# Kernel tuning notes

Hardware: AMD Instinct MI355X
Metric: run time of the kernel (lower is better)

Reference implementation:

```python
import jax, jax.numpy as jnp
import numpy as np

N_NODES = 500_000
N_EDGES = 16_000_000


def setup_inputs() -> dict:
    key = jax.random.key(0)
    ks = jax.random.split(key, 8)
    x = jax.random.normal(ks[0], (N_NODES, 10), dtype=jnp.float32)
    edge_index = jax.random.randint(ks[1], (2, N_EDGES), 0, N_NODES, dtype=jnp.int32)
    # PyG-style init scale ~ 1/sqrt(fan_in)
    Wl1 = jax.random.normal(ks[2], (5, 10), dtype=jnp.float32) / np.sqrt(10)
    Wr1 = jax.random.normal(ks[3], (5, 10), dtype=jnp.float32) / np.sqrt(10)
    b1 = jnp.zeros((5,), jnp.float32)
    Wl_mid = jax.random.normal(ks[4], (8, 5, 5), dtype=jnp.float32) / np.sqrt(5)
    Wr_mid = jax.random.normal(ks[5], (8, 5, 5), dtype=jnp.float32) / np.sqrt(5)
    b_mid = jnp.zeros((8, 5), jnp.float32)
    Wl10 = jax.random.normal(ks[6], (1, 5), dtype=jnp.float32) / np.sqrt(5)
    Wr10 = jax.random.normal(ks[7], (1, 5), dtype=jnp.float32) / np.sqrt(5)
    b10 = jnp.zeros((1,), jnp.float32)
    return dict(x=x, edge_index=edge_index, Wl1=Wl1, Wr1=Wr1, b1=b1,
                Wl_mid=Wl_mid, Wr_mid=Wr_mid, b_mid=b_mid,
                Wl10=Wl10, Wr10=Wr10, b10=b10)


def _mean_aggregate(h, src, dst):
    # scatter-mean of source features onto destination nodes
    s = jax.ops.segment_sum(h[src], dst, num_segments=N_NODES)
    cnt = jax.ops.segment_sum(jnp.ones((src.shape[0], 1), h.dtype), dst,
                              num_segments=N_NODES)
    return s / jnp.maximum(cnt, 1.0)


def _sage_conv(h, src, dst, Wl, Wr, b):
    # out = lin_l(mean_neighbors) + lin_r(h); bias belongs to lin_l (PyG default)
    agg = _mean_aggregate(h, src, dst)
    return agg @ Wl.T + h @ Wr.T + b


def reference(x, edge_index, Wl1, Wr1, b1, Wl_mid, Wr_mid, b_mid, Wl10, Wr10, b10):
    src, dst = edge_index[0], edge_index[1]
    h = jax.nn.relu(_sage_conv(x, src, dst, Wl1, Wr1, b1))

    def step(h, layer_params):
        Wl, Wr, b = layer_params
        h = jax.nn.relu(_sage_conv(h, src, dst, Wl, Wr, b))
        return h, None

    h, _ = jax.lax.scan(step, h, (Wl_mid, Wr_mid, b_mid))
    out = _sage_conv(h, src, dst, Wl10, Wr10, b10)  # [N, 1], no relu on last
    return out
```

## Files before the change

kernel.cpp:

```cpp
#include <hip/hip_runtime.h>

constexpr int NN = 500000;
constexpr int NE = 16000000;
constexpr int BN = 512;
constexpr int NBUCK = (NN + BN - 1) / BN;
constexpr int NSLICE = 8;
constexpr int NKEY = NSLICE * BN;
constexpr int CAPA = 17408;
constexpr int PAIR_CAP = 5120;
constexpr int TILE_A = 16384;
constexpr int NTILE_A = (NE + TILE_A - 1) / TILE_A;
constexpr int NB_NODE = (NN + 255) / 256;

typedef int int4v __attribute__((ext_vector_type(4)));

__device__ __forceinline__ unsigned bfr(float x) {
    unsigned u = __float_as_uint(x);
    u += 0x7fffu + ((u >> 16) & 1u);
    return u >> 16;
}
__device__ __forceinline__ float bfl(unsigned u) { return __uint_as_float(u << 16); }
__device__ __forceinline__ float bfh(unsigned u) { return __uint_as_float(u & 0xffff0000u); }

__global__ void __launch_bounds__(1024, 8) passA(const int* __restrict__ src,
                                                 const int* __restrict__ dst,
                                                 int* __restrict__ gcnt,
                                                 int* __restrict__ storeA) {
    __shared__ int hist[1024];
    __shared__ int lbase[1024];
    __shared__ int lcur[1024];
    __shared__ int gbase[1024];
    __shared__ int stage[TILE_A];
    const int tid = threadIdx.x;
    const int base = blockIdx.x * TILE_A;
    const int nt = min(TILE_A, NE - base);
    hist[tid] = 0;
    __syncthreads();
    for (int i = tid; i < nt; i += 1024)
        atomicAdd(&hist[dst[base + i] >> 9], 1);
    __syncthreads();
    const int cnt = hist[tid];
    lbase[tid] = cnt;
    __syncthreads();
    for (int off = 1; off < 1024; off <<= 1) {
        int add = (tid >= off) ? lbase[tid - off] : 0;
        __syncthreads();
        lbase[tid] += add;
        __syncthreads();
    }
    const int lb = lbase[tid] - cnt;
    lcur[tid] = lb;
    if (tid < NBUCK && cnt > 0) {
        int g = atomicAdd(&gcnt[tid], cnt);
        gbase[tid] = tid * CAPA + g;
    }
    __syncthreads();
    lbase[tid] = lb;
    for (int i = tid; i < nt; i += 1024) {
        int d = dst[base + i];
        int s = src[base + i];
        int p = atomicAdd(&lcur[d >> 9], 1);
        stage[p] = (s << 9) | (d & 511);
    }
    __syncthreads();
    const int wid = tid >> 6, lane = tid & 63;
    for (int b = wid; b < NBUCK; b += 16) {
        int c = hist[b];
        if (c == 0) continue;
        int l0 = lbase[b];
        int g0 = gbase[b];
        int wl = min(c, (b + 1) * CAPA - g0);
        for (int j = lane; j < wl; j += 64)
            storeA[g0 + j] = stage[l0 + j];
    }
}

__global__ void __launch_bounds__(512) passB(const int* __restrict__ gcnt,
                                             const int* __restrict__ storeA,
                                             int* __restrict__ sortedB,
                                             float* __restrict__ inv,
                                             int* __restrict__ soff) {
    __shared__ int hist[NKEY];
    __shared__ int sc[512];
    __shared__ int stage[CAPA];
    const int bkt = blockIdx.x;
    const int tid = threadIdx.x;
#pragma unroll
    for (int u = 0; u < NKEY / 512; ++u) hist[tid + u * 512] = 0;
    __syncthreads();
    const int n = min(gcnt[bkt], CAPA);
    const int* bs = storeA + (size_t)bkt * CAPA;
    const int n4 = n & ~3;
    for (int k = tid * 4; k < n4; k += 2048) {
        int4v e4 = *(const int4v*)(bs + k);
#pragma unroll
        for (int u = 0; u < 4; ++u) {
            int e = e4[u];
            int key = ((e >> 26) << 10) | ((e & 511) << 1) | ((e >> 25) & 1);
            atomicAdd(&hist[key], 1);
        }
    }
    for (int k = n4 + tid; k < n; k += 512) {
        int e = bs[k];
        int key = ((e >> 26) << 10) | ((e & 511) << 1) | ((e >> 25) & 1);
        atomicAdd(&hist[key], 1);
    }
    __syncthreads();
    {
        int node = bkt * BN + tid;
        if (node < NN) {
            int c = 0;
#pragma unroll
            for (int p = 0; p < 4; ++p)
#pragma unroll
                for (int q = 0; q < 2; ++q)
                    c += hist[(p << 10) | (tid << 1) | q];
            inv[node] = 1.0f / fmaxf((float)c, 1.0f);
        }
    }
    int v[NKEY / 512];
    int sum = 0;
#pragma unroll
    for (int u = 0; u < NKEY / 512; ++u) {
        v[u] = hist[tid * (NKEY / 512) + u];
        sum += v[u];
    }
    sc[tid] = sum;
    __syncthreads();
    for (int off = 1; off < 512; off <<= 1) {
        int add = (tid >= off) ? sc[tid - off] : 0;
        __syncthreads();
        sc[tid] += add;
        __syncthreads();
    }
    int run = sc[tid] - sum;
    if ((tid & 127) == 0) soff[bkt * 9 + (tid >> 7)] = bkt * CAPA + run;
    if (tid == 511) soff[bkt * 9 + 4] = bkt * CAPA + n;
#pragma unroll
    for (int u = 0; u < NKEY / 512; ++u) {
        hist[tid * (NKEY / 512) + u] = run;
        run += v[u];
    }
    __syncthreads();
    for (int k = tid * 4; k < n4; k += 2048) {
        int4v e4 = *(const int4v*)(bs + k);
#pragma unroll
        for (int u = 0; u < 4; ++u) {
            int e = e4[u];
            int key = ((e >> 26) << 10) | ((e & 511) << 1) | ((e >> 25) & 1);
            int p = atomicAdd(&hist[key], 1);
            stage[p] = e;
        }
    }
    for (int k = n4 + tid; k < n; k += 512) {
        int e = bs[k];
        int key = ((e >> 26) << 10) | ((e & 511) << 1) | ((e >> 25) & 1);
        int p = atomicAdd(&hist[key], 1);
        stage[p] = e;
    }
    __syncthreads();
    int* ob = sortedB + (size_t)bkt * CAPA;
    for (int k = tid * 4; k < n4; k += 2048)
        *(int4v*)(ob + k) = *(const int4v*)(stage + k);
    for (int k = n4 + tid; k < n; k += 512)
        ob[k] = stage[k];
}

__global__ void __launch_bounds__(256) transform0(const float* __restrict__ x,
                                                  const float* __restrict__ Wl1,
                                                  uint4* __restrict__ t16) {
    int i = blockIdx.x * 256 + threadIdx.x;
    if (i >= NN) return;
    float xi[10];
#pragma unroll
    for (int k = 0; k < 10; ++k) xi[k] = x[i * 10 + k];
    float v[5];
#pragma unroll
    for (int j = 0; j < 5; ++j) {
        float a = 0.f;
#pragma unroll
        for (int k = 0; k < 10; ++k) a += xi[k] * Wl1[j * 10 + k];
        v[j] = a;
    }
    uint4 w;
    w.x = bfr(v[0]) | (bfr(v[1]) << 16);
    w.y = bfr(v[2]) | (bfr(v[3]) << 16);
    w.z = bfr(v[4]);
    w.w = 0;
    t16[i] = w;
}

__device__ __forceinline__ void process_range5_lds(const int* eds,
                                                   int k, const int ke,
                                                   const uint4* __restrict__ t16,
                                                   float* __restrict__ acc) {
    int cur = -1;
    float a0 = 0, a1 = 0, a2 = 0, a3 = 0, a4 = 0;
    auto flush = [&]() {
        if (cur >= 0) {
            float* p = &acc[cur * 5];
            atomicAdd(p + 0, a0); atomicAdd(p + 1, a1); atomicAdd(p + 2, a2);
            atomicAdd(p + 3, a3); atomicAdd(p + 4, a4);
        }
    };
    auto edge = [&](int e, uint4 w) {
        int d = e & 511;
        if (d != cur) { flush(); cur = d; a0 = a1 = a2 = a3 = a4 = 0.f; }
        a0 += bfl(w.x); a1 += bfh(w.x); a2 += bfl(w.y); a3 += bfh(w.y); a4 += bfl(w.z);
    };
    while (k < ke && (k & 3)) {
        int e = eds[k];
        edge(e, t16[e >> 9]);
        ++k;
    }
    for (; k + 3 < ke; k += 4) {
        int4v e4 = *(const int4v*)(eds + k);
        uint4 w0 = t16[e4.x >> 9];
        uint4 w1 = t16[e4.y >> 9];
        uint4 w2 = t16[e4.z >> 9];
        uint4 w3 = t16[e4.w >> 9];
        edge(e4.x, w0); edge(e4.y, w1); edge(e4.z, w2); edge(e4.w, w3);
    }
    for (; k < ke; ++k) {
        int e = eds[k];
        edge(e, t16[e >> 9]);
    }
    flush();
}

template <int FIN, int FNEXT>
__global__ void __launch_bounds__(512, 8) layer_fused(const int* __restrict__ soff,
                                                      const int* __restrict__ sorted,
                                                      const uint4* __restrict__ t16,
                                                      const float* __restrict__ hin,
                                                      const float* __restrict__ Wr,
                                                      const float* __restrict__ b,
                                                      const float* __restrict__ Wln,
                                                      const float* __restrict__ inv,
                                                      float* __restrict__ hout,
                                                      uint4* __restrict__ tn16,
                                                      float* __restrict__ tnP) {
    __shared__ float acc[BN * 5];
    __shared__ int eds[PAIR_CAP];
    const int bkt = blockIdx.x;
    const int tid = threadIdx.x;
    for (int k = tid; k < BN * 5; k += 512) acc[k] = 0.f;
#pragma unroll
    for (int p = 0; p < 4; ++p) {
        const int beg = soff[bkt * 9 + p];
        const int n = min(soff[bkt * 9 + p + 1] - beg, PAIR_CAP);
#pragma unroll 4
        for (int k = tid; k < n; k += 512)
            eds[k] = __builtin_nontemporal_load(sorted + beg + k);
        __syncthreads();
        const int c = (n + 511) >> 9;
        const int k = tid * c;
        const int ke = min(k + c, n);
        if (k < ke) process_range5_lds(eds, k, ke, t16, acc);
        __syncthreads();
    }

    int node = bkt * BN + tid;
    if (node >= NN) return;
    float iv = inv[node];
    float vin[FIN];
#pragma unroll
    for (int kk = 0; kk < FIN; ++kk) vin[kk] = hin[(size_t)node * FIN + kk];
    float ho[5];
#pragma unroll
    for (int jo = 0; jo < 5; ++jo) {
        float v = acc[tid * 5 + jo] * iv + b[jo];
#pragma unroll
        for (int kk = 0; kk < FIN; ++kk) v += vin[kk] * Wr[jo * FIN + kk];
        v = fmaxf(v, 0.f);
        hout[(size_t)node * 5 + jo] = v;
        ho[jo] = v;
    }
    if constexpr (FNEXT == 5) {
        float tv[5];
#pragma unroll
        for (int j2 = 0; j2 < 5; ++j2) {
            float v = 0.f;
#pragma unroll
            for (int jo = 0; jo < 5; ++jo) v += ho[jo] * Wln[j2 * 5 + jo];
            tv[j2] = v;
        }
        uint4 w;
        w.x = bfr(tv[0]) | (bfr(tv[1]) << 16);
        w.y = bfr(tv[2]) | (bfr(tv[3]) << 16);
        w.z = bfr(tv[4]);
        w.w = 0;
        tn16[node] = w;
    } else {
        float v = 0.f;
#pragma unroll
        for (int jo = 0; jo < 5; ++jo) v += ho[jo] * Wln[jo];
        tnP[node] = v;
    }
}

__global__ void __launch_bounds__(512, 4) final_layer(const int* __restrict__ soff,
                                                      const int* __restrict__ sorted,
                                                      const float* __restrict__ t,
                                                      const float* __restrict__ hin,
                                                      const float* __restrict__ Wr,
                                                      const float* __restrict__ b,
                                                      const float* __restrict__ inv,
                                                      float* __restrict__ out) {
    __shared__ float acc[BN];
    __shared__ int eds[CAPA];
    const int bkt = blockIdx.x;
    const int tid = threadIdx.x;
    const int base = bkt * CAPA;
    const int n = soff[bkt * 9 + 4] - base;
    if (tid < BN) acc[tid] = 0.f;
    const int sn4 = n & ~3;
    for (int k = tid * 4; k < sn4; k += 2048)
        *(int4v*)(eds + k) = __builtin_nontemporal_load((const int4v*)(sorted + base + k));
    for (int k = sn4 + tid; k < n; k += 512)
        eds[k] = sorted[base + k];
    __syncthreads();
    int c = (n + 511) >> 9;
    int k = tid * c;
    const int ke = min(k + c, n);
    int cur = -1;
    float a0 = 0.f;
    auto flush = [&]() { if (cur >= 0) atomicAdd(&acc[cur], a0); };
    auto edge = [&](int e, float q) {
        int d = e & 511;
        if (d != cur) { flush(); cur = d; a0 = 0.f; }
        a0 += q;
    };
    int kk = k;
    while (kk < ke && (kk & 3)) { int e = eds[kk]; edge(e, t[e >> 9]); ++kk; }
    for (; kk + 3 < ke; kk += 4) {
        int4v e4 = *(const int4v*)(eds + kk);
        float q0 = t[e4.x >> 9], q1 = t[e4.y >> 9], q2 = t[e4.z >> 9], q3 = t[e4.w >> 9];
        edge(e4.x, q0); edge(e4.y, q1); edge(e4.z, q2); edge(e4.w, q3);
    }
    for (; kk < ke; ++kk) { int e = eds[kk]; edge(e, t[e >> 9]); }
    flush();
    __syncthreads();
    int node = bkt * BN + tid;
    if (node >= NN) return;
    float v = acc[tid] * inv[node] + b[0];
#pragma unroll
    for (int kq = 0; kq < 5; ++kq) v += hin[(size_t)node * 5 + kq] * Wr[kq];
    out[node] = v;
}

extern "C" void kernel_launch(void* const* d_in, const int* in_sizes, int n_in,
                              void* d_out, int out_size, void* d_ws, size_t ws_size,
                              hipStream_t stream) {
    (void)in_sizes; (void)n_in; (void)out_size; (void)ws_size;
    const float* x    = (const float*)d_in[0];
    const int*   ei   = (const int*)d_in[1];
    const float* Wl1  = (const float*)d_in[2];
    const float* Wr1  = (const float*)d_in[3];
    const float* b1   = (const float*)d_in[4];
    const float* Wlm  = (const float*)d_in[5];
    const float* Wrm  = (const float*)d_in[6];
    const float* bm   = (const float*)d_in[7];
    const float* Wl10 = (const float*)d_in[8];
    const float* Wr10 = (const float*)d_in[9];
    const float* b10  = (const float*)d_in[10];
    float* out = (float*)d_out;

    const int* src = ei;
    const int* dst = ei + NE;

    int* wsI = (int*)d_ws;
    int*   gcnt    = wsI;
    int*   soff    = wsI + 1024;
    int*   sortedB = wsI + 10240;
    float* inv     = (float*)(wsI + 17017856);
    int*   storeA  = wsI + 20019200;
    uint4* tA = (uint4*)(wsI + 20019200);
    uint4* tB = (uint4*)(wsI + 22019200);
    float* tP = (float*)(wsI + 24019200);
    float* hA = (float*)(wsI + 24519424);
    float* hB = (float*)(wsI + 27020032);

    dim3 gb(NBUCK);
    dim3 tb(512);

    hipMemsetAsync(gcnt, 0, 1024 * sizeof(int), stream);
    passA<<<dim3(NTILE_A), dim3(1024), 0, stream>>>(src, dst, gcnt, storeA);
    passB<<<gb, tb, 0, stream>>>(gcnt, storeA, sortedB, inv, soff);

    transform0<<<dim3(NB_NODE), dim3(256), 0, stream>>>(x, Wl1, tA);
    layer_fused<10, 5><<<gb, tb, 0, stream>>>(soff, sortedB, tA,
                                              x, Wr1, b1, Wlm, inv, hA, tB, nullptr);

    const uint4* tcur = tB; uint4* tnxt = tA;
    const float* hcur = hA; float* hnext = hB;
    for (int mi = 0; mi < 7; ++mi) {
        layer_fused<5, 5><<<gb, tb, 0, stream>>>(soff, sortedB, tcur,
                                                 hcur, Wrm + mi * 25, bm + mi * 5,
                                                 Wlm + (mi + 1) * 25, inv, hnext,
                                                 tnxt, nullptr);
        const uint4* tt = tcur; tcur = tnxt; tnxt = (uint4*)tt;
        const float* th = hcur; hcur = hnext; hnext = (float*)th;
    }
    layer_fused<5, 1><<<gb, tb, 0, stream>>>(soff, sortedB, tcur,
                                             hcur, Wrm + 7 * 25, bm + 7 * 5,
                                             Wl10, inv, hnext, nullptr, tP);
    final_layer<<<gb, tb, 0, stream>>>(soff, sortedB, tP, hnext, Wr10, b10, inv, out);
}
```

Measured before the change: 1.558 ms.

## Double-buffer edge slices in layer_fused and slice final_layer into smaller LDS chunks

In the fused middle layer, the edge list for the next slice is prefetched into registers while the current slice is processed from a second LDS buffer, so global-load latency overlaps the gather/accumulate work. The final layer now walks the same four per-slice segments with a small PAIR_CAP LDS buffer instead of one large CAPA buffer, and its launch bound rises to 8 blocks/CU to raise occupancy. The trade-off is ten extra registers per thread plus doubled LDS in layer_fused, which may lower occupancy there, and extra barriers in the final layer.

Result: slower. 1.590 ms (+2.1%).

```diff
diff --git a/kernel.cpp b/kernel.cpp
--- a/kernel.cpp
+++ b/kernel.cpp
@@ -241,22 +241,43 @@
                                                       uint4* __restrict__ tn16,
                                                       float* __restrict__ tnP) {
     __shared__ float acc[BN * 5];
-    __shared__ int eds[PAIR_CAP];
+    __shared__ int eds[2][PAIR_CAP];
     const int bkt = blockIdx.x;
     const int tid = threadIdx.x;
     for (int k = tid; k < BN * 5; k += 512) acc[k] = 0.f;
+    {
+        const int beg = soff[bkt * 9 + 0];
+        const int n0 = min(soff[bkt * 9 + 1] - beg, PAIR_CAP);
+        for (int k = tid; k < n0; k += 512)
+            eds[0][k] = __builtin_nontemporal_load(sorted + beg + k);
+    }
+    __syncthreads();
 #pragma unroll
     for (int p = 0; p < 4; ++p) {
-        const int beg = soff[bkt * 9 + p];
-        const int n = min(soff[bkt * 9 + p + 1] - beg, PAIR_CAP);
-#pragma unroll 4
-        for (int k = tid; k < n; k += 512)
-            eds[k] = __builtin_nontemporal_load(sorted + beg + k);
-        __syncthreads();
+        const int cur = p & 1;
+        const int n = min(soff[bkt * 9 + p + 1] - soff[bkt * 9 + p], PAIR_CAP);
+        int r[10];
+        int nn = 0, begn = 0;
+        if (p < 3) {
+            begn = soff[bkt * 9 + p + 1];
+            nn = min(soff[bkt * 9 + p + 2] - begn, PAIR_CAP);
+#pragma unroll
+            for (int j = 0; j < 10; ++j) {
+                int k = tid + j * 512;
+                if (k < nn) r[j] = __builtin_nontemporal_load(sorted + begn + k);
+            }
+        }
         const int c = (n + 511) >> 9;
-        const int k = tid * c;
-        const int ke = min(k + c, n);
-        if (k < ke) process_range5_lds(eds, k, ke, t16, acc);
+        const int k0 = tid * c;
+        const int ke = min(k0 + c, n);
+        if (k0 < ke) process_range5_lds(&eds[cur][0], k0, ke, t16, acc);
+        if (p < 3) {
+#pragma unroll
+            for (int j = 0; j < 10; ++j) {
+                int k = tid + j * 512;
+                if (k < nn) eds[cur ^ 1][k] = r[j];
+            }
+        }
         __syncthreads();
     }
 
@@ -299,7 +320,7 @@
     }
 }
 
-__global__ void __launch_bounds__(512, 4) final_layer(const int* __restrict__ soff,
+__global__ void __launch_bounds__(512, 8) final_layer(const int* __restrict__ soff,
                                                       const int* __restrict__ sorted,
                                                       const float* __restrict__ t,
                                                       const float* __restrict__ hin,
@@ -308,39 +329,38 @@
                                                       const float* __restrict__ inv,
                                                       float* __restrict__ out) {
     __shared__ float acc[BN];
-    __shared__ int eds[CAPA];
+    __shared__ int eds[PAIR_CAP];
     const int bkt = blockIdx.x;
     const int tid = threadIdx.x;
-    const int base = bkt * CAPA;
-    const int n = soff[bkt * 9 + 4] - base;
-    if (tid < BN) acc[tid] = 0.f;
-    const int sn4 = n & ~3;
-    for (int k = tid * 4; k < sn4; k += 2048)
-        *(int4v*)(eds + k) = __builtin_nontemporal_load((const int4v*)(sorted + base + k));
-    for (int k = sn4 + tid; k < n; k += 512)
-        eds[k] = sorted[base + k];
-    __syncthreads();
-    int c = (n + 511) >> 9;
-    int k = tid * c;
-    const int ke = min(k + c, n);
-    int cur = -1;
-    float a0 = 0.f;
-    auto flush = [&]() { if (cur >= 0) atomicAdd(&acc[cur], a0); };
-    auto edge = [&](int e, float q) {
-        int d = e & 511;
-        if (d != cur) { flush(); cur = d; a0 = 0.f; }
-        a0 += q;
-    };
-    int kk = k;
-    while (kk < ke && (kk & 3)) { int e = eds[kk]; edge(e, t[e >> 9]); ++kk; }
-    for (; kk + 3 < ke; kk += 4) {
-        int4v e4 = *(const int4v*)(eds + kk);
-        float q0 = t[e4.x >> 9], q1 = t[e4.y >> 9], q2 = t[e4.z >> 9], q3 = t[e4.w >> 9];
-        edge(e4.x, q0); edge(e4.y, q1); edge(e4.z, q2); edge(e4.w, q3);
-    }
-    for (; kk < ke; ++kk) { int e = eds[kk]; edge(e, t[e >> 9]); }
-    flush();
-    __syncthreads();
+    acc[tid] = 0.f;
+#pragma unroll
+    for (int p = 0; p < 4; ++p) {
+        const int beg = soff[bkt * 9 + p];
+        const int n = min(soff[bkt * 9 + p + 1] - beg, PAIR_CAP);
+        for (int k = tid; k < n; k += 512)
+            eds[k] = __builtin_nontemporal_load(sorted + beg + k);
+        __syncthreads();
+        const int c = (n + 511) >> 9;
+        int kk = tid * c;
+        const int ke = min(kk + c, n);
+        int cur = -1;
+        float a0 = 0.f;
+        auto flush = [&]() { if (cur >= 0) atomicAdd(&acc[cur], a0); };
+        auto edge = [&](int e, float q) {
+            int d = e & 511;
+            if (d != cur) { flush(); cur = d; a0 = 0.f; }
+            a0 += q;
+        };
+        while (kk < ke && (kk & 3)) { int e = eds[kk]; edge(e, t[e >> 9]); ++kk; }
+        for (; kk + 3 < ke; kk += 4) {
+            int4v e4 = *(const int4v*)(eds + kk);
+            float q0 = t[e4.x >> 9], q1 = t[e4.y >> 9], q2 = t[e4.z >> 9], q3 = t[e4.w >> 9];
+            edge(e4.x, q0); edge(e4.y, q1); edge(e4.z, q2); edge(e4.w, q3);
+        }
+        for (; kk < ke; ++kk) { int e = eds[kk]; edge(e, t[e >> 9]); }
+        flush();
+        __syncthreads();
+    }
     int node = bkt * BN + tid;
     if (node >= NN) return;
     float v = acc[tid] * inv[node] + b[0];
```
